# Kernel tuning notes

Measured on AMD Instinct MI355X. Metric: run time of the kernel, lower is better.

Reference implementation:

```python
import math
import jax, jax.numpy as jnp
from jax import lax
import numpy as np

THETA = 10.0      # spiking threshold
TAU_SR = 10.0     # SRM (psp) alpha-kernel time constant
TAU_REF = 1.0     # refractory alpha-kernel time constant
SCALE_REF = 2.0   # refractory scale (kernel = -scaleRef*theta*alpha)
TAU_RHO = 1.0     # surrogate-gradient width
TS = 1.0          # simulation time step


def _alpha_filter_scan(x, tau, extra_input_fn=None):
    """Causal convolution along last (time) axis with alpha kernel
    k[n] = (n*Ts/tau) * exp(1 - n*Ts/tau)  (k[0] = 0),
    implemented exactly as a 2-state linear recurrence.
    x: [N, C, T] -> out: [N, C, T]."""
    d = jnp.float32(math.exp(-TS / tau))
    c = jnp.float32(math.e * TS / tau)
    xT = jnp.moveaxis(x, -1, 0)  # [T, N, C]

    def step(carry, xt):
        p, a = carry
        a = d * (a + p)          # alpha response from inputs up to t-1
        p = d * p + xt           # pure exponential state
        return (p, a), a * c

    z = jnp.zeros_like(xT[0])
    _, out = lax.scan(step, (z, z), xT)
    return jnp.moveaxis(out, 0, -1)


def psp(x):
    return _alpha_filter_scan(x, TAU_SR)


@jax.custom_vjp
def spike_fn(v):
    # Heaviside threshold on (membrane - theta)
    return (v >= 0).astype(v.dtype)

def _spike_fwd(v):
    return spike_fn(v), v

def _spike_bwd(v, g):
    # SLAYER surrogate gradient: exponential pdf around threshold
    grad = (1.0 / TAU_RHO) * jnp.exp(-jnp.abs(v) / TAU_RHO)
    return (g * grad,)

spike_fn.defvjp(_spike_fwd, _spike_bwd)


def spike_layer(u_in):
    """Threshold-and-refract over time. u_in: [N, C, T] psp potentials.
    Refractory response = -scaleRef*theta * alpha_{tauRef}(past spikes)."""
    d = jnp.float32(math.exp(-TS / TAU_REF))
    c = jnp.float32(math.e * TS / TAU_REF)
    ref_scale = jnp.float32(-SCALE_REF * THETA)
    uT = jnp.moveaxis(u_in, -1, 0)  # [T, N, C]

    def step(carry, ut):
        p, a = carry
        a = d * (a + p)                      # refractory potential at t
        u = ut + c * a                       # membrane potential
        s = spike_fn(u - THETA)              # spikes (0/1)
        p = d * p + ref_scale * s            # inject refractory impulse
        return (p, a), s

    z = jnp.zeros_like(uT[0])
    _, s = lax.scan(step, (z, z), uT)
    return jnp.moveaxis(s, 0, -1)


def setup_inputs() -> dict:
    key = jax.random.key(0)
    k1, k2, k3 = jax.random.split(key, 3)
    N, I, H, O, T = 64, 256, 1024, 18, 500
    # Bernoulli(0.1) input spikes
    spike_input = (jax.random.uniform(k1, (N, I, T)) < 0.1).astype(jnp.float32)
    W1 = jax.random.normal(k2, (H, I), dtype=jnp.float32) * (1.0 / math.sqrt(I))
    W2 = jax.random.normal(k3, (O, H), dtype=jnp.float32) * (1.0 / math.sqrt(H))
    return {"spike_input": spike_input, "W1": W1, "W2": W2}


def reference(spike_input, W1, W2):
    # layer 1: dense (per-timestep linear) -> psp -> spike
    y1 = jnp.einsum('nit,hi->nht', spike_input, W1)
    s1 = spike_layer(psp(y1))
    # layer 2
    y2 = jnp.einsum('nht,oh->not', s1, W2)
    s2 = spike_layer(psp(y2))
    return s2
```

## Files before the change

kernel.cpp:

```cpp
#include <hip/hip_runtime.h>


#define NN 64
#define II 256
#define HH 1024
#define OO 18
#define TT 500

#define D_SR 0.9048374180359595f
#define C_SR 0.27182818284590454f
#define D_RF 0.36787944117144233f
#define C_RF 2.718281828459045f
#define THETA 10.0f
#define REFS (-20.0f)

typedef _Float16 f16;
typedef _Float16 f16x2 __attribute__((ext_vector_type(2)));
typedef _Float16 f16x8 __attribute__((ext_vector_type(8)));
typedef float f32x4 __attribute__((ext_vector_type(4)));

__device__ __forceinline__ void gl2lds16(const void* g, void* l) {
    __builtin_amdgcn_global_load_lds(
        (const __attribute__((address_space(1))) void*)g,
        (__attribute__((address_space(3))) void*)l, 16, 0, 0);
}

__launch_bounds__(256)
__global__ void prep_x(const float* __restrict__ X, f16* __restrict__ Xb) {
    __shared__ float tile[64][65];
    const int n = blockIdx.z, i0 = blockIdx.y * 64, t0 = blockIdx.x * 64;
    const int tx = threadIdx.x & 63, q = threadIdx.x >> 6;
    const float* Xn = X + (size_t)n * II * TT;
#pragma unroll 4
    for (int j = 0; j < 16; ++j) {
        int il = j * 4 + q;
        int t = t0 + tx;
        tile[il][tx] = (t < TT) ? Xn[(size_t)(i0 + il) * TT + t] : 0.f;
    }
    __syncthreads();
#pragma unroll 4
    for (int j = 0; j < 16; ++j) {
        int tl = j * 4 + q;
        int t = t0 + tl;
        if (t < TT)
            Xb[((size_t)n * TT + t) * II + i0 + tx] = (f16)tile[tx][tl];
    }
}

__launch_bounds__(256)
__global__ void prep_w1(const float* __restrict__ W1, f16* __restrict__ Wh,
                        f16* __restrict__ Wl) {
    int idx = blockIdx.x * 256 + threadIdx.x;
    float w = W1[idx];
    f16 h = (f16)w;
    f16 l = (f16)(w - (float)h);
    Wh[idx] = h;
    Wl[idx] = l;
}

__launch_bounds__(256)
__global__ void prep_w2(const float* __restrict__ W2, f16* __restrict__ Wh,
                        f16* __restrict__ Wl) {
    int idx = blockIdx.x * 256 + threadIdx.x;
    int o = idx >> 10;
    float w = (o < OO) ? W2[idx] : 0.f;
    f16 h = (f16)w;
    f16 l = (f16)(w - (float)h);
    Wh[idx] = h;
    Wl[idx] = l;
}

__launch_bounds__(256)
__global__ void gemm1_scan1(const f16* __restrict__ Xb, const f16* __restrict__ Wh,
                            const f16* __restrict__ Wl, f16* __restrict__ S1) {
    __shared__ __align__(16) char smem[128 * 132 * 4];
    float* yb = (float*)smem;

    const int tid = threadIdx.x;
    const int wave = tid >> 6, lane = tid & 63;

    const int f = blockIdx.y * 8 + blockIdx.x;
    const int x = f & 7, g = f >> 3;
    const int n = x * 8 + (g & 7);
    const int ht = g >> 3;
    const int h0g = ht * 128;

    const int rbl = wave * 32 + (lane >> 2);
    const int koff = (lane & 3) * 8;
    const f16* gBh0 = Wh + (size_t)(h0g + rbl) * II + koff;
    const f16* gBl0 = Wl + (size_t)(h0g + rbl) * II + koff;

    const int wm = wave & 1, wn = wave >> 1;
    const int fr = lane & 15, kq = lane >> 4;

    float p1 = 0.f, a1 = 0.f, p2 = 0.f, a2 = 0.f;

    for (int c = 0; c < 4; ++c) {
        const int t0 = c * 128;
        const int TCe = (TT - t0 < 128) ? (TT - t0) : 128;

        int r0 = rbl;      if (r0 > TCe - 1) r0 = TCe - 1;
        int r1 = rbl + 16; if (r1 > TCe - 1) r1 = TCe - 1;
        const f16* gA0 = Xb + ((size_t)n * TT + t0 + r0) * II + koff;
        const f16* gA1 = Xb + ((size_t)n * TT + t0 + r1) * II + koff;

        auto stage = [&](int kk2, int b) {
            f16* As_b = (f16*)(smem + b * 24576);
            f16* Bh_b = As_b + 4096;
            f16* Bl_b = As_b + 8192;
            const int ko = kk2 * 32;
            gl2lds16(gA0 + ko, As_b + wave * 1024);
            gl2lds16(gA1 + ko, As_b + wave * 1024 + 512);
            gl2lds16(gBh0 + ko, Bh_b + wave * 1024);
            gl2lds16(gBh0 + 16 * II + ko, Bh_b + wave * 1024 + 512);
            gl2lds16(gBl0 + ko, Bl_b + wave * 1024);
            gl2lds16(gBl0 + 16 * II + ko, Bl_b + wave * 1024 + 512);
        };

        stage(0, 0);

        f32x4 acc[4][4] = {};
        for (int kk = 0; kk < 8; ++kk) {
            __syncthreads();
            if (kk < 7) stage(kk + 1, (kk + 1) & 1);

            const f16* As_b = (const f16*)(smem + (kk & 1) * 24576);
            const f16* Bh_b = As_b + 4096;
            const f16* Bl_b = As_b + 8192;

            f16x8 av[4], bhv[4], blv[4];
#pragma unroll
            for (int i = 0; i < 4; ++i) {
                av[i]  = *(const f16x8*)(As_b + (wm * 64 + i * 16 + fr) * 32 + kq * 8);
                bhv[i] = *(const f16x8*)(Bh_b + (wn * 64 + i * 16 + fr) * 32 + kq * 8);
                blv[i] = *(const f16x8*)(Bl_b + (wn * 64 + i * 16 + fr) * 32 + kq * 8);
            }
#pragma unroll
            for (int i = 0; i < 4; ++i)
#pragma unroll
                for (int j = 0; j < 4; ++j) {
                    acc[i][j] = __builtin_amdgcn_mfma_f32_16x16x32_f16(av[i], bhv[j], acc[i][j], 0, 0, 0);
                    acc[i][j] = __builtin_amdgcn_mfma_f32_16x16x32_f16(av[i], blv[j], acc[i][j], 0, 0, 0);
                }
        }
        __syncthreads();

#pragma unroll
        for (int i = 0; i < 4; ++i)
#pragma unroll
            for (int j = 0; j < 4; ++j) {
                int tr = wm * 64 + i * 16 + kq * 4;
                int hc = wn * 64 + j * 16 + fr;
#pragma unroll
                for (int r = 0; r < 4; ++r)
                    yb[(tr + r) * 132 + hc] = acc[i][j][r];
            }
        __syncthreads();

        if (tid < 128) {
            f16* sq = S1 + ((size_t)n * TT + t0) * HH + h0g + tid;
            float rb_[8];
#pragma unroll
            for (int j = 0; j < 8; ++j) rb_[j] = yb[j * 132 + tid];
            int t = 0;
            for (; t + 8 <= TCe; t += 8) {
#pragma unroll
                for (int j = 0; j < 8; ++j) {
                    float xv = rb_[j];
                    int tn = t + j + 8;
                    rb_[j] = (tn < TCe) ? yb[tn * 132 + tid] : 0.f;
                    a1 = D_SR * (a1 + p1);
                    p1 = D_SR * p1 + xv;
                    float ut = C_SR * a1;
                    a2 = D_RF * (a2 + p2);
                    float u = ut + C_RF * a2;
                    float s = (u >= THETA) ? 1.0f : 0.0f;
                    p2 = D_RF * p2 + REFS * s;
                    sq[(size_t)(t + j) * HH] = (f16)s;
                }
            }
            int rem = TCe - t;
#pragma unroll
            for (int j = 0; j < 8; ++j) {
                if (j < rem) {
                    float xv = rb_[j];
                    a1 = D_SR * (a1 + p1);
                    p1 = D_SR * p1 + xv;
                    float ut = C_SR * a1;
                    a2 = D_RF * (a2 + p2);
                    float u = ut + C_RF * a2;
                    float s = (u >= THETA) ? 1.0f : 0.0f;
                    p2 = D_RF * p2 + REFS * s;
                    sq[(size_t)(t + j) * HH] = (f16)s;
                }
            }
        }
        __syncthreads();
    }
}

__launch_bounds__(256)
__global__ void gemm2_mfma(const f16* __restrict__ S1, const f16* __restrict__ W2h,
                           const f16* __restrict__ W2l, float* __restrict__ Y2) {
    __shared__ __align__(16) f16 As[2][128 * 32];
    __shared__ __align__(16) f16 Bh[2][32 * 32];
    __shared__ __align__(16) f16 Bl[2][32 * 32];

    const int tid = threadIdx.x;
    const int wave = tid >> 6, lane = tid & 63;
    const int m0 = blockIdx.x * 128;
    const int fr = lane & 15, kq = lane >> 4;

    const f16* gA0 = S1 + (size_t)(m0 + wave * 32 + (lane >> 2)) * HH + (lane & 3) * 8;
    const f16* gA1 = gA0 + (size_t)16 * HH;
    const f16* gB = (wave < 2 ? W2h : W2l) + (size_t)((wave & 1) * 16 + (lane >> 2)) * HH + (lane & 3) * 8;

    auto stage = [&](int kk2, int b) {
        const int ko = kk2 * 32;
        gl2lds16(gA0 + ko, &As[b][wave * 1024]);
        gl2lds16(gA1 + ko, &As[b][wave * 1024 + 512]);
        gl2lds16(gB + ko, (wave < 2 ? &Bh[b][0] : &Bl[b][0]) + (wave & 1) * 512);
    };

    stage(0, 0);

    f32x4 acc[2][2] = {};
    for (int kk = 0; kk < HH / 32; ++kk) {
        __syncthreads();
        if (kk < HH / 32 - 1) stage(kk + 1, (kk + 1) & 1);
        const int b = kk & 1;

        f16x8 a[2], bh[2], bl[2];
#pragma unroll
        for (int i = 0; i < 2; ++i) {
            a[i]  = *(const f16x8*)(&As[b][(wave * 32 + i * 16 + fr) * 32 + kq * 8]);
            bh[i] = *(const f16x8*)(&Bh[b][(i * 16 + fr) * 32 + kq * 8]);
            bl[i] = *(const f16x8*)(&Bl[b][(i * 16 + fr) * 32 + kq * 8]);
        }
#pragma unroll
        for (int i = 0; i < 2; ++i)
#pragma unroll
            for (int j = 0; j < 2; ++j) {
                acc[i][j] = __builtin_amdgcn_mfma_f32_16x16x32_f16(a[i], bh[j], acc[i][j], 0, 0, 0);
                acc[i][j] = __builtin_amdgcn_mfma_f32_16x16x32_f16(a[i], bl[j], acc[i][j], 0, 0, 0);
            }
    }

#pragma unroll
    for (int i = 0; i < 2; ++i)
#pragma unroll
        for (int j = 0; j < 2; ++j) {
            int rbase = m0 + wave * 32 + i * 16 + kq * 4;
            int cc = j * 16 + fr;
            float* p = Y2 + (size_t)rbase * 32 + cc;
#pragma unroll
            for (int r = 0; r < 4; ++r)
                p[(size_t)r * 32] = acc[i][j][r];
        }
}

__launch_bounds__(256)
__global__ void scan2_k(const float* __restrict__ Y2, float* __restrict__ Out) {
    __shared__ float yc[250 * 32];
    __shared__ float sb[OO * TT];
    const int n = blockIdx.x, tid = threadIdx.x;

    float p1 = 0.f, a1 = 0.f, p2 = 0.f, a2 = 0.f;

    for (int half = 0; half < 2; ++half) {
        const float4* src = (const float4*)(Y2 + ((size_t)n * TT + half * 250) * 32);
        float4* dst = (float4*)yc;
        for (int i = tid; i < 2000; i += 256) dst[i] = src[i];
        __syncthreads();

        if (tid < 32) {
            float rb_[8];
#pragma unroll
            for (int j = 0; j < 8; ++j) rb_[j] = yc[j * 32 + tid];
            int t = 0;
            for (; t + 8 <= 250; t += 8) {
#pragma unroll
                for (int j = 0; j < 8; ++j) {
                    float xv = rb_[j];
                    int tn = t + j + 8;
                    rb_[j] = (tn < 250) ? yc[tn * 32 + tid] : 0.f;
                    a1 = D_SR * (a1 + p1);
                    p1 = D_SR * p1 + xv;
                    float ut = C_SR * a1;
                    a2 = D_RF * (a2 + p2);
                    float u = ut + C_RF * a2;
                    float s = (u >= THETA) ? 1.0f : 0.0f;
                    p2 = D_RF * p2 + REFS * s;
                    if (tid < OO) sb[tid * TT + half * 250 + t + j] = s;
                }
            }
#pragma unroll
            for (int j = 0; j < 8; ++j) {
                if (t + j < 250) {
                    float xv = rb_[j];
                    a1 = D_SR * (a1 + p1);
                    p1 = D_SR * p1 + xv;
                    float ut = C_SR * a1;
                    a2 = D_RF * (a2 + p2);
                    float u = ut + C_RF * a2;
                    float s = (u >= THETA) ? 1.0f : 0.0f;
                    p2 = D_RF * p2 + REFS * s;
                    if (tid < OO) sb[tid * TT + half * 250 + t + j] = s;
                }
            }
        }
        __syncthreads();
    }

    float* on = Out + (size_t)n * OO * TT;
    for (int e = tid; e < OO * TT; e += 256) on[e] = sb[e];
}

extern "C" void kernel_launch(void* const* d_in, const int* in_sizes, int n_in,
                              void* d_out, int out_size, void* d_ws, size_t ws_size,
                              hipStream_t stream) {
    const float* X  = (const float*)d_in[0];
    const float* W1 = (const float*)d_in[1];
    const float* W2 = (const float*)d_in[2];
    float* out = (float*)d_out;

    const size_t s_s1 = (size_t)NN * TT * HH * 2;
    const size_t s_Xb = (size_t)NN * TT * II * 2;
    const size_t s_W  = (size_t)HH * II * 2;
    const size_t s_W2 = (size_t)32 * HH * 2;

    char* w = (char*)d_ws;
    f16*   s1b = (f16*)w;  w += s_s1;
    f16*   Xb  = (f16*)w;  w += s_Xb;
    f16*   W1h = (f16*)w;  w += s_W;
    f16*   W1l = (f16*)w;  w += s_W;
    f16*   W2h = (f16*)w;  w += s_W2;
    f16*   W2l = (f16*)w;  w += s_W2;
    float* y2  = (float*)w;

    prep_x<<<dim3(8, 4, NN), 256, 0, stream>>>(X, Xb);
    prep_w1<<<(HH * II) / 256, 256, 0, stream>>>(W1, W1h, W1l);
    prep_w2<<<(32 * HH) / 256, 256, 0, stream>>>(W2, W2h, W2l);

    gemm1_scan1<<<dim3(8, NN), 256, 0, stream>>>(Xb, W1h, W1l, s1b);

    gemm2_mfma<<<(NN * TT) / 128, 256, 0, stream>>>(s1b, W2h, W2l, y2);
    scan2_k<<<NN, 256, 0, stream>>>(y2, out);
}
```

Measured before the change: 196.1 us.

## Load GEMM1 operands directly from global into registers, dropping LDS staging

Replaces the double-buffered global-to-LDS staging of A, Wh and Wl tiles in gemm1_scan1 with per-lane direct global loads into registers, software-pipelined across k-steps. This removes the per-k-step __syncthreads barriers and the LDS round trip. In exchange, each wave reloads operands that other waves share, so global and L2 traffic rises, and the doubled register buffers raise register pressure. The loads are also less coalesced, each lane reading 16 bytes from a different row.

```diff
diff --git a/kernel.cpp b/kernel.cpp
--- a/kernel.cpp
+++ b/kernel.cpp
@@ -73,8 +73,7 @@
 __launch_bounds__(256)
 __global__ void gemm1_scan1(const f16* __restrict__ Xb, const f16* __restrict__ Wh,
                             const f16* __restrict__ Wl, f16* __restrict__ S1) {
-    __shared__ __align__(16) char smem[128 * 132 * 4];
-    float* yb = (float*)smem;
+    __shared__ float yb[128 * 132];
 
     const int tid = threadIdx.x;
     const int wave = tid >> 6, lane = tid & 63;
@@ -85,13 +84,17 @@
     const int ht = g >> 3;
     const int h0g = ht * 128;
 
-    const int rbl = wave * 32 + (lane >> 2);
-    const int koff = (lane & 3) * 8;
-    const f16* gBh0 = Wh + (size_t)(h0g + rbl) * II + koff;
-    const f16* gBl0 = Wl + (size_t)(h0g + rbl) * II + koff;
-
     const int wm = wave & 1, wn = wave >> 1;
     const int fr = lane & 15, kq = lane >> 4;
+
+    const f16* bhp[4];
+    const f16* blp[4];
+#pragma unroll
+    for (int j = 0; j < 4; ++j) {
+        int hrow = h0g + wn * 64 + j * 16 + fr;
+        bhp[j] = Wh + (size_t)hrow * II + kq * 8;
+        blp[j] = Wl + (size_t)hrow * II + kq * 8;
+    }
 
     float p1 = 0.f, a1 = 0.f, p2 = 0.f, a2 = 0.f;
 
@@ -99,51 +102,42 @@
         const int t0 = c * 128;
         const int TCe = (TT - t0 < 128) ? (TT - t0) : 128;
 
-        int r0 = rbl;      if (r0 > TCe - 1) r0 = TCe - 1;
-        int r1 = rbl + 16; if (r1 > TCe - 1) r1 = TCe - 1;
-        const f16* gA0 = Xb + ((size_t)n * TT + t0 + r0) * II + koff;
-        const f16* gA1 = Xb + ((size_t)n * TT + t0 + r1) * II + koff;
-
-        auto stage = [&](int kk2, int b) {
-            f16* As_b = (f16*)(smem + b * 24576);
-            f16* Bh_b = As_b + 4096;
-            f16* Bl_b = As_b + 8192;
-            const int ko = kk2 * 32;
-            gl2lds16(gA0 + ko, As_b + wave * 1024);
-            gl2lds16(gA1 + ko, As_b + wave * 1024 + 512);
-            gl2lds16(gBh0 + ko, Bh_b + wave * 1024);
-            gl2lds16(gBh0 + 16 * II + ko, Bh_b + wave * 1024 + 512);
-            gl2lds16(gBl0 + ko, Bl_b + wave * 1024);
-            gl2lds16(gBl0 + 16 * II + ko, Bl_b + wave * 1024 + 512);
-        };
-
-        stage(0, 0);
+        const f16* ap[4];
+#pragma unroll
+        for (int i = 0; i < 4; ++i) {
+            int ar = wm * 64 + i * 16 + fr;
+            if (ar > TCe - 1) ar = TCe - 1;
+            ap[i] = Xb + ((size_t)n * TT + t0 + ar) * II + kq * 8;
+        }
 
         f32x4 acc[4][4] = {};
+        f16x8 av[2][4], bhv[2][4], blv[2][4];
+#pragma unroll
+        for (int i = 0; i < 4; ++i) {
+            av[0][i]  = *(const f16x8*)(ap[i]);
+            bhv[0][i] = *(const f16x8*)(bhp[i]);
+            blv[0][i] = *(const f16x8*)(blp[i]);
+        }
+#pragma unroll
         for (int kk = 0; kk < 8; ++kk) {
-            __syncthreads();
-            if (kk < 7) stage(kk + 1, (kk + 1) & 1);
-
-            const f16* As_b = (const f16*)(smem + (kk & 1) * 24576);
-            const f16* Bh_b = As_b + 4096;
-            const f16* Bl_b = As_b + 8192;
-
-            f16x8 av[4], bhv[4], blv[4];
-#pragma unroll
-            for (int i = 0; i < 4; ++i) {
-                av[i]  = *(const f16x8*)(As_b + (wm * 64 + i * 16 + fr) * 32 + kq * 8);
-                bhv[i] = *(const f16x8*)(Bh_b + (wn * 64 + i * 16 + fr) * 32 + kq * 8);
-                blv[i] = *(const f16x8*)(Bl_b + (wn * 64 + i * 16 + fr) * 32 + kq * 8);
+            const int cur = kk & 1, nxt = cur ^ 1;
+            if (kk < 7) {
+                const int ko = (kk + 1) * 32;
+#pragma unroll
+                for (int i = 0; i < 4; ++i) {
+                    av[nxt][i]  = *(const f16x8*)(ap[i] + ko);
+                    bhv[nxt][i] = *(const f16x8*)(bhp[i] + ko);
+                    blv[nxt][i] = *(const f16x8*)(blp[i] + ko);
+                }
             }
 #pragma unroll
             for (int i = 0; i < 4; ++i)
 #pragma unroll
                 for (int j = 0; j < 4; ++j) {
-                    acc[i][j] = __builtin_amdgcn_mfma_f32_16x16x32_f16(av[i], bhv[j], acc[i][j], 0, 0, 0);
-                    acc[i][j] = __builtin_amdgcn_mfma_f32_16x16x32_f16(av[i], blv[j], acc[i][j], 0, 0, 0);
-                }
-        }
-        __syncthreads();
+                    acc[i][j] = __builtin_amdgcn_mfma_f32_16x16x32_f16(av[cur][i], bhv[cur][j], acc[i][j], 0, 0, 0);
+                    acc[i][j] = __builtin_amdgcn_mfma_f32_16x16x32_f16(av[cur][i], blv[cur][j], acc[i][j], 0, 0, 0);
+                }
+        }
 
 #pragma unroll
         for (int i = 0; i < 4; ++i)
```

New measurement: 269.9 us. 37.6% more time.
